# Kernel tuning notes

Hardware: AMD Instinct MI355X
Metric: run time of the kernel (lower is better)

The kernel has to match this reference:

```python
import jax, jax.numpy as jnp
import numpy as np

B, C, T = 8, 1024, 2048
CI = C // 2
BN_EPS = 1e-5


def setup_inputs() -> dict:
    key = jax.random.key(0)
    ks = jax.random.split(key, 12)
    sc_in = 1.0 / np.sqrt(C)
    sc_ci = 1.0 / np.sqrt(CI)
    return {
        "x": jax.random.normal(ks[0], (B, C, T), dtype=jnp.float32),
        "Wq_w": jax.random.normal(ks[1], (CI, C), dtype=jnp.float32) * sc_in,
        "Wq_b": jax.random.normal(ks[2], (CI,), dtype=jnp.float32) * 0.02,
        "Wk_w": jax.random.normal(ks[3], (CI, C), dtype=jnp.float32) * sc_in,
        "Wk_b": jax.random.normal(ks[4], (CI,), dtype=jnp.float32) * 0.02,
        "Wv_w": jax.random.normal(ks[5], (CI, C), dtype=jnp.float32) * sc_in,
        "Wv_b": jax.random.normal(ks[6], (CI,), dtype=jnp.float32) * 0.02,
        "Wo_w": jax.random.normal(ks[7], (C, CI), dtype=jnp.float32) * sc_ci,
        "Wo_b": jax.random.normal(ks[8], (C,), dtype=jnp.float32) * 0.02,
        "gamma": jax.random.normal(ks[9], (C,), dtype=jnp.float32) * 0.1 + 1.0,
        "beta": jax.random.normal(ks[10], (C,), dtype=jnp.float32) * 0.02,
    }


def reference(x, Wq_w, Wq_b, Wk_w, Wk_b, Wv_w, Wv_b, Wo_w, Wo_b, gamma, beta):
    # 1x1 Conv1d projections == channel-wise linear maps
    q = jnp.einsum('oc,bct->bto', Wq_w, x) + Wq_b          # [B, T, Ci]
    k = jnp.einsum('oc,bct->bot', Wk_w, x) + Wk_b[:, None]  # [B, Ci, T]
    v = jnp.einsum('oc,bct->bto', Wv_w, x) + Wv_b          # [B, T, Ci]

    s = jnp.einsum('bqc,bck->bqk', q, k)                   # [B, Tq, Tk], unscaled
    sim = jax.nn.softmax(s, axis=-2)                        # softmax over QUERY axis
    y = jnp.einsum('bqk,bkc->bcq', sim, v)                  # [B, Ci, T]

    wy = jnp.einsum('oc,bct->bot', Wo_w, y) + Wo_b[:, None]  # [B, C, T]

    # BatchNorm1d in training mode: stats over (batch, time) per channel
    mean = jnp.mean(wy, axis=(0, 2), keepdims=True)
    var = jnp.var(wy, axis=(0, 2), keepdims=True)
    wy_bn = (wy - mean) * jax.lax.rsqrt(var + BN_EPS)
    wy_bn = wy_bn * gamma[None, :, None] + beta[None, :, None]

    return wy_bn + x
```

## Files before the change

### kernel.cpp

```cpp
#include <hip/hip_runtime.h>
#include <hip/hip_fp16.h>

typedef _Float16 f16;
typedef f16 f16x8 __attribute__((ext_vector_type(8)));
typedef f16 f16x4 __attribute__((ext_vector_type(4)));
typedef float f32x4 __attribute__((ext_vector_type(4)));

constexpr int Bb = 8, Cc = 1024, Tt = 2048, Ci = 512;
constexpr float BN_EPS = 1e-5f;

__device__ __forceinline__ void gload16(const f16* g, f16* l) {
  __builtin_amdgcn_global_load_lds(
      (const __attribute__((address_space(1))) void*)g,
      (__attribute__((address_space(3))) void*)l, 16, 0, 0);
}

__global__ __launch_bounds__(256)
void cvt_kernel(const float* __restrict__ src, f16* __restrict__ dst, int n4) {
  int i = blockIdx.x * blockDim.x + threadIdx.x;
  if (i < n4) {
    float4 v = *((const float4*)src + i);
    f16x4 h;
    h[0] = (f16)v.x; h[1] = (f16)v.y; h[2] = (f16)v.z; h[3] = (f16)v.w;
    *((f16x4*)dst + i) = h;
  }
}

__global__ __launch_bounds__(256)
void cvtT_kernel(const float* __restrict__ x, f16* __restrict__ xT) {
  __shared__ float tile[64][68];
  const int b = blockIdx.z, c0 = blockIdx.y * 64, t0 = blockIdx.x * 64;
  const int tid = threadIdx.x;
  const float* xp = x + ((long)b * Cc + c0) * Tt + t0;
  {
    int r = tid >> 4, c4 = (tid & 15) * 4;
    #pragma unroll
    for (int it = 0; it < 4; it++) {
      float4 v = *(const float4*)(xp + (long)(r + it * 16) * Tt + c4);
      *(float4*)&tile[r + it * 16][c4] = v;
    }
  }
  __syncthreads();
  f16* op = xT + ((long)b * Tt + t0) * Cc + c0;
  {
    int c8 = (tid & 7) * 8;
    #pragma unroll
    for (int it = 0; it < 2; it++) {
      int t = (tid >> 3) + it * 32;
      f16x8 o;
      #pragma unroll
      for (int jj = 0; jj < 8; jj++) o[jj] = (f16)tile[c8 + jj][t];
      *(f16x8*)(op + (long)t * Cc + c8) = o;
    }
  }
}

template<int BIAS_MODE>
__global__ __launch_bounds__(512, 2)
void gemm8p(const f16* __restrict__ A, const f16* __restrict__ B,
            f16* __restrict__ C, const float* __restrict__ bias,
            int K, int lda, int ldb, int ldc, long sA, long sB, long sC)
{
  extern __shared__ f16 lds[];
  constexpr int TILE_A = 256 * 64;
  constexpr int TILE_B = 128 * 64;
  constexpr int TILE   = TILE_A + TILE_B;

  const int tid = threadIdx.x, lane = tid & 63, wv = tid >> 6;
  const int bm0 = blockIdx.y * 256, bn0 = blockIdx.x * 128;
  const int wm = (wv >> 1) * 64, wn = (wv & 1) * 64;
  const f16* Ab = A + (long)blockIdx.z * sA + (long)bm0 * lda;
  const f16* Bt = B + (long)blockIdx.z * sB + (long)bn0 * ldb;
  C += (long)blockIdx.z * sC;

  const int r16 = lane & 15, khi = lane >> 4;
  const int sw = (r16 & 7) << 4;

  auto stA = [&](int slot, int k0, int r) {
    int L = (r * 512 + tid) * 16;
    int G = L ^ (((L >> 7) & 7) << 4);
    gload16(Ab + (long)(G >> 7) * lda + k0 + ((G & 127) >> 1),
            lds + (long)slot * TILE + (r * 512 + wv * 64) * 8);
  };
  auto stB = [&](int slot, int k0, int r) {
    int L = (r * 512 + tid) * 16;
    int G = L ^ (((L >> 7) & 7) << 4);
    gload16(Bt + (long)(G >> 7) * ldb + k0 + ((G & 127) >> 1),
            lds + (long)slot * TILE + TILE_A + (r * 512 + wv * 64) * 8);
  };

  f32x4 acc[4][4] = {};
  const int nt = K >> 6;

  #pragma unroll
  for (int r = 0; r < 4; r++) stA(0, 0, r);
  #pragma unroll
  for (int r = 0; r < 2; r++) stB(0, 0, r);
  #pragma unroll
  for (int r = 0; r < 4; r++) stA(1, 64, r);
  #pragma unroll
  for (int r = 0; r < 2; r++) stB(1, 64, r);
  asm volatile("s_waitcnt vmcnt(6)" ::: "memory");
  __builtin_amdgcn_s_barrier();

  for (int t = 0; t < nt; t++) {
    const int slot = t % 3;
    const int nslot = (t + 2) % 3;
    const int k2 = (t + 2) << 6;
    const bool st = (t + 2) < nt;
    const char* baseA = (const char*)(lds + (long)slot * TILE);
    const char* baseB = (const char*)(lds + (long)slot * TILE + TILE_A);

    if (st) {
      stA(nslot, k2, 0); stA(nslot, k2, 1); stA(nslot, k2, 2); stA(nslot, k2, 3);
      stB(nslot, k2, 0); stB(nslot, k2, 1);
    }

    f16x8 af0[4], bf0[4], af1[4], bf1[4];
    #pragma unroll
    for (int mi = 0; mi < 4; mi++)
      af0[mi] = *(const f16x8*)(baseA + (((wm + mi * 16 + r16) * 128 + khi * 16) ^ sw));
    #pragma unroll
    for (int nj = 0; nj < 4; nj++)
      bf0[nj] = *(const f16x8*)(baseB + (((wn + nj * 16 + r16) * 128 + khi * 16) ^ sw));
    #pragma unroll
    for (int mi = 0; mi < 4; mi++)
      af1[mi] = *(const f16x8*)(baseA + (((wm + mi * 16 + r16) * 128 + 64 + khi * 16) ^ sw));
    #pragma unroll
    for (int nj = 0; nj < 4; nj++)
      bf1[nj] = *(const f16x8*)(baseB + (((wn + nj * 16 + r16) * 128 + 64 + khi * 16) ^ sw));

    __builtin_amdgcn_s_setprio(1);
    #pragma unroll
    for (int mi = 0; mi < 4; mi++)
      #pragma unroll
      for (int nj = 0; nj < 4; nj++)
        acc[mi][nj] = __builtin_amdgcn_mfma_f32_16x16x32_f16(af0[mi], bf0[nj], acc[mi][nj], 0, 0, 0);
    #pragma unroll
    for (int mi = 0; mi < 4; mi++)
      #pragma unroll
      for (int nj = 0; nj < 4; nj++)
        acc[mi][nj] = __builtin_amdgcn_mfma_f32_16x16x32_f16(af1[mi], bf1[nj], acc[mi][nj], 0, 0, 0);
    __builtin_amdgcn_s_setprio(0);

    __builtin_amdgcn_sched_barrier(0);
    if (st) asm volatile("s_waitcnt vmcnt(6)" ::: "memory");
    else    asm volatile("s_waitcnt vmcnt(0)" ::: "memory");
    __builtin_amdgcn_s_barrier();
  }

  const int rg = khi * 4;
  #pragma unroll
  for (int mi = 0; mi < 4; mi++) {
    const int row = bm0 + wm + mi * 16 + rg;
    #pragma unroll
    for (int nj = 0; nj < 4; nj++) {
      const int col = bn0 + wn + nj * 16 + r16;
      const float bn_ = (BIAS_MODE == 2) ? bias[col] : 0.0f;
      #pragma unroll
      for (int r = 0; r < 4; r++) {
        float v = acc[mi][nj][r] + ((BIAS_MODE == 1) ? bias[row + r] : bn_);
        C[(long)(row + r) * ldc + col] = (f16)v;
      }
    }
  }
}

__global__ __launch_bounds__(256)
void rowstat_kernel(const f16* __restrict__ S, float* __restrict__ maxs,
                    float* __restrict__ sums) {
  __shared__ float red[8];
  const int tid = threadIdx.x;
  const f16* p = S + (long)blockIdx.x * Tt;
  f16x8 v = *((const f16x8*)p + tid);
  float f[8];
  float mx = -3e38f;
  #pragma unroll
  for (int j = 0; j < 8; j++) { f[j] = (float)v[j]; mx = fmaxf(mx, f[j]); }
  #pragma unroll
  for (int off = 1; off < 64; off <<= 1) mx = fmaxf(mx, __shfl_xor(mx, off));
  const int w = tid >> 6;
  if ((tid & 63) == 0) red[w] = mx;
  __syncthreads();
  mx = fmaxf(fmaxf(red[0], red[1]), fmaxf(red[2], red[3]));
  float sum = 0.f;
  #pragma unroll
  for (int j = 0; j < 8; j++) sum += __expf(f[j] - mx);
  #pragma unroll
  for (int off = 1; off < 64; off <<= 1) sum += __shfl_xor(sum, off);
  __syncthreads();
  if ((tid & 63) == 0) red[4 + w] = sum;
  __syncthreads();
  if (tid == 0) {
    maxs[blockIdx.x] = mx;
    sums[blockIdx.x] = (red[4] + red[5]) + (red[6] + red[7]);
  }
}

__global__ __launch_bounds__(256)
void transnorm_kernel(const f16* __restrict__ St, const float* __restrict__ maxs,
                      const float* __restrict__ sums, f16* __restrict__ P) {
  __shared__ f16 tile[64][72];
  __shared__ float rm[64], ri[64];
  const int b = blockIdx.z, kt0 = blockIdx.y * 64, q0 = blockIdx.x * 64;
  const int tid = threadIdx.x;
  if (tid < 64) {
    rm[tid] = maxs[(long)b * Tt + kt0 + tid];
    ri[tid] = 1.0f / sums[(long)b * Tt + kt0 + tid];
  }
  const f16* Sp = St + ((long)b * Tt + kt0) * Tt + q0;
  {
    int r = tid >> 3, c8 = (tid & 7) * 8;
    #pragma unroll
    for (int it = 0; it < 2; it++) {
      f16x8 v = *(const f16x8*)(Sp + (long)(r + it * 32) * Tt + c8);
      *(f16x8*)&tile[r + it * 32][c8] = v;
    }
  }
  __syncthreads();
  f16* Pp = P + ((long)b * Tt + q0) * Tt + kt0;
  {
    int kt8 = (tid & 7) * 8;
    #pragma unroll
    for (int it = 0; it < 2; it++) {
      int q = (tid >> 3) + it * 32;
      f16x8 o;
      #pragma unroll
      for (int jj = 0; jj < 8; jj++) {
        int kt = kt8 + jj;
        o[jj] = (f16)(__expf((float)tile[kt][q] - rm[kt]) * ri[kt]);
      }
      *(f16x8*)(Pp + (long)q * Tt + kt8) = o;
    }
  }
}

__global__ __launch_bounds__(256)
void bnstat_kernel(const f16* __restrict__ wy, float* __restrict__ bsum,
                   float* __restrict__ bsq) {
  const int c = blockIdx.x, tid = threadIdx.x;
  float s1 = 0.f, s2 = 0.f;
  for (int b = 0; b < Bb; b++) {
    f16x8 v = *((const f16x8*)(wy + ((long)b * Cc + c) * Tt) + tid);
    #pragma unroll
    for (int jj = 0; jj < 8; jj++) { float f = (float)v[jj]; s1 += f; s2 += f * f; }
  }
  #pragma unroll
  for (int off = 1; off < 64; off <<= 1) {
    s1 += __shfl_xor(s1, off);
    s2 += __shfl_xor(s2, off);
  }
  __shared__ float l1[4], l2[4];
  const int w = tid >> 6;
  if ((tid & 63) == 0) { l1[w] = s1; l2[w] = s2; }
  __syncthreads();
  if (tid == 0) {
    bsum[c] = (l1[0] + l1[1]) + (l1[2] + l1[3]);
    bsq[c]  = (l2[0] + l2[1]) + (l2[2] + l2[3]);
  }
}

__global__ __launch_bounds__(256)
void final_kernel(const f16* __restrict__ wy, const float* __restrict__ x,
                  const float* __restrict__ gamma, const float* __restrict__ beta,
                  const float* __restrict__ bsum, const float* __restrict__ bsq,
                  float* __restrict__ out)
{
  long i = ((long)blockIdx.x * blockDim.x + threadIdx.x) * 4;
  int c = (int)((i >> 11) & (Cc - 1));
  const float cnt = (float)Bb * (float)Tt;
  float mean = bsum[c] / cnt;
  float var  = bsq[c] / cnt - mean * mean;
  float sc = rsqrtf(var + BN_EPS) * gamma[c];
  float sh = beta[c] - mean * sc;
  f16x4 w = *(const f16x4*)(wy + i);
  float4 xv = *(const float4*)(x + i);
  float4 o;
  o.x = (float)w[0] * sc + sh + xv.x;
  o.y = (float)w[1] * sc + sh + xv.y;
  o.z = (float)w[2] * sc + sh + xv.z;
  o.w = (float)w[3] * sc + sh + xv.w;
  *(float4*)(out + i) = o;
}

extern "C" void kernel_launch(void* const* d_in, const int* in_sizes, int n_in,
                              void* d_out, int out_size, void* d_ws, size_t ws_size,
                              hipStream_t stream) {
  const float* x    = (const float*)d_in[0];
  const float* Wq_w = (const float*)d_in[1];
  const float* Wq_b = (const float*)d_in[2];
  const float* Wk_w = (const float*)d_in[3];
  const float* Wk_b = (const float*)d_in[4];
  const float* Wv_w = (const float*)d_in[5];
  const float* Wv_b = (const float*)d_in[6];
  const float* Wo_w = (const float*)d_in[7];
  const float* Wo_b = (const float*)d_in[8];
  const float* gamma = (const float*)d_in[9];
  const float* beta  = (const float*)d_in[10];
  float* out = (float*)d_out;

  constexpr long SZ_XT = (long)Bb * Tt * Cc;
  constexpr long SZ_Q  = (long)Bb * Tt * Ci;
  constexpr long SZ_S  = (long)Bb * Tt * Tt;
  constexpr long SZ_W  = (long)Ci * Cc;

  f16* ws = (f16*)d_ws;
  f16* xT = ws;
  f16* P  = ws;
  f16* Qm = ws + SZ_XT;
  f16* Km = Qm + SZ_Q;
  f16* Vt = Km + SZ_Q;
  f16* St = Vt + SZ_Q;
  f16* wq = St + SZ_S;
  f16* wk = wq + SZ_W;
  f16* wv = wk + SZ_W;
  f16* wo = wv + SZ_W;
  f16* Y  = wo + SZ_W;
  f16* wy = Y + SZ_Q;
  float* maxs = (float*)(wy + SZ_XT);
  float* sums = maxs + (long)Bb * Tt;
  float* bsum = sums + (long)Bb * Tt;
  float* bsq  = bsum + Cc;

  constexpr int LDSB = (256 * 64 + 128 * 64) * 3 * 2;
  hipFuncSetAttribute(reinterpret_cast<const void*>(gemm8p<0>),
                      hipFuncAttributeMaxDynamicSharedMemorySize, LDSB);
  hipFuncSetAttribute(reinterpret_cast<const void*>(gemm8p<1>),
                      hipFuncAttributeMaxDynamicSharedMemorySize, LDSB);
  hipFuncSetAttribute(reinterpret_cast<const void*>(gemm8p<2>),
                      hipFuncAttributeMaxDynamicSharedMemorySize, LDSB);

  cvt_kernel<<<(int)(SZ_W / 4 / 256), 256, 0, stream>>>(Wq_w, wq, (int)(SZ_W / 4));
  cvt_kernel<<<(int)(SZ_W / 4 / 256), 256, 0, stream>>>(Wk_w, wk, (int)(SZ_W / 4));
  cvt_kernel<<<(int)(SZ_W / 4 / 256), 256, 0, stream>>>(Wv_w, wv, (int)(SZ_W / 4));
  cvt_kernel<<<(int)(SZ_W / 4 / 256), 256, 0, stream>>>(Wo_w, wo, (int)(SZ_W / 4));
  cvtT_kernel<<<dim3(Tt / 64, Cc / 64, Bb), 256, 0, stream>>>(x, xT);

  gemm8p<2><<<dim3(Ci / 128, Tt / 256, Bb), 512, LDSB, stream>>>(
      xT, wq, Qm, Wq_b, Cc, Cc, Cc, Ci, (long)Tt * Cc, 0, (long)Tt * Ci);
  gemm8p<2><<<dim3(Ci / 128, Tt / 256, Bb), 512, LDSB, stream>>>(
      xT, wk, Km, Wk_b, Cc, Cc, Cc, Ci, (long)Tt * Cc, 0, (long)Tt * Ci);
  gemm8p<1><<<dim3(Tt / 128, Ci / 256, Bb), 512, LDSB, stream>>>(
      wv, xT, Vt, Wv_b, Cc, Cc, Cc, Tt, 0, (long)Tt * Cc, (long)Ci * Tt);

  gemm8p<0><<<dim3(Tt / 128, Tt / 256, Bb), 512, LDSB, stream>>>(
      Km, Qm, St, nullptr, Ci, Ci, Ci, Tt, (long)Tt * Ci, (long)Tt * Ci, (long)Tt * Tt);

  rowstat_kernel<<<Bb * Tt, 256, 0, stream>>>(St, maxs, sums);
  transnorm_kernel<<<dim3(Tt / 64, Tt / 64, Bb), 256, 0, stream>>>(St, maxs, sums, P);

  gemm8p<0><<<dim3(Ci / 128, Tt / 256, Bb), 512, LDSB, stream>>>(
      P, Vt, Y, nullptr, Tt, Tt, Tt, Ci, (long)Tt * Tt, (long)Ci * Tt, (long)Tt * Ci);

  gemm8p<1><<<dim3(Tt / 128, Cc / 256, Bb), 512, LDSB, stream>>>(
      wo, Y, wy, Wo_b, Ci, Ci, Ci, Tt, 0, (long)Tt * Ci, (long)Cc * Tt);

  bnstat_kernel<<<Cc, 256, 0, stream>>>(wy, bsum, bsq);
  final_kernel<<<(int)(SZ_XT / 4 / 256), 256, 0, stream>>>(
      wy, x, gamma, beta, bsum, bsq, out);
}
```

Before: 300.6 us.

## Fuse softmax stats and BN stats into GEMM epilogues, merge Q/K projection

Computes S as Q·K^T so softmax over the query axis becomes per-column. The column max is produced by atomics in the GEMM epilogue, and a column-sum kernel exponentiates S in place. Normalisation moves onto V through a per-key scale instead of a separate transpose-normalise pass. The Q and K projections are merged into one GEMM, BatchNorm sums are accumulated with atomics in the output-projection epilogue, and blocks are remapped for XCD locality. Together these remove the rowstat, transnorm and bnstat passes and their extra traffic over the large S matrix, at the cost of atomic contention and a strided column-walking pass.

```diff
diff --git a/kernel.cpp b/kernel.cpp
--- a/kernel.cpp
+++ b/kernel.cpp
@@ -55,23 +55,32 @@
   }
 }
 
-template<int BIAS_MODE>
+template<int BIAS_MODE, bool DO_MAX, bool DO_BN>
 __global__ __launch_bounds__(512, 2)
 void gemm8p(const f16* __restrict__ A, const f16* __restrict__ B,
             f16* __restrict__ C, const float* __restrict__ bias,
-            int K, int lda, int ldb, int ldc, long sA, long sB, long sC)
+            unsigned* __restrict__ gmax, float* __restrict__ bnsum,
+            float* __restrict__ bnsq,
+            int K, int lda, int ldb, int ldc, long sA, long sB, long sC,
+            int nx, int ny)
 {
   extern __shared__ f16 lds[];
   constexpr int TILE_A = 256 * 64;
   constexpr int TILE_B = 128 * 64;
   constexpr int TILE   = TILE_A + TILE_B;
 
+  const int per = gridDim.x >> 3;
+  const int nid = (blockIdx.x & 7) * per + (blockIdx.x >> 3);
+  const int bz = nid / (nx * ny);
+  const int rem = nid - bz * nx * ny;
+  const int by = rem / nx, bx = rem - by * nx;
+
   const int tid = threadIdx.x, lane = tid & 63, wv = tid >> 6;
-  const int bm0 = blockIdx.y * 256, bn0 = blockIdx.x * 128;
+  const int bm0 = by * 256, bn0 = bx * 128;
   const int wm = (wv >> 1) * 64, wn = (wv & 1) * 64;
-  const f16* Ab = A + (long)blockIdx.z * sA + (long)bm0 * lda;
-  const f16* Bt = B + (long)blockIdx.z * sB + (long)bn0 * ldb;
-  C += (long)blockIdx.z * sC;
+  const f16* Ab = A + (long)bz * sA + (long)bm0 * lda;
+  const f16* Bt = B + (long)bz * sB + (long)bn0 * ldb;
+  C += (long)bz * sC;
 
   const int r16 = lane & 15, khi = lane >> 4;
   const int sw = (r16 & 7) << 4;
@@ -118,29 +127,24 @@
 
     f16x8 af0[4], bf0[4], af1[4], bf1[4];
     #pragma unroll
-    for (int mi = 0; mi < 4; mi++)
-      af0[mi] = *(const f16x8*)(baseA + (((wm + mi * 16 + r16) * 128 + khi * 16) ^ sw));
-    #pragma unroll
-    for (int nj = 0; nj < 4; nj++)
-      bf0[nj] = *(const f16x8*)(baseB + (((wn + nj * 16 + r16) * 128 + khi * 16) ^ sw));
-    #pragma unroll
-    for (int mi = 0; mi < 4; mi++)
-      af1[mi] = *(const f16x8*)(baseA + (((wm + mi * 16 + r16) * 128 + 64 + khi * 16) ^ sw));
-    #pragma unroll
-    for (int nj = 0; nj < 4; nj++)
-      bf1[nj] = *(const f16x8*)(baseB + (((wn + nj * 16 + r16) * 128 + 64 + khi * 16) ^ sw));
+    for (int i = 0; i < 4; i++) {
+      af0[i] = *(const f16x8*)(baseA + (((wm + i * 16 + r16) * 128 + khi * 16) ^ sw));
+      af1[i] = *(const f16x8*)(baseA + (((wm + i * 16 + r16) * 128 + 64 + khi * 16) ^ sw));
+    }
+    #pragma unroll
+    for (int j = 0; j < 4; j++) {
+      bf0[j] = *(const f16x8*)(baseB + (((wn + j * 16 + r16) * 128 + khi * 16) ^ sw));
+      bf1[j] = *(const f16x8*)(baseB + (((wn + j * 16 + r16) * 128 + 64 + khi * 16) ^ sw));
+    }
 
     __builtin_amdgcn_s_setprio(1);
     #pragma unroll
-    for (int mi = 0; mi < 4; mi++)
+    for (int i = 0; i < 4; i++)
       #pragma unroll
-      for (int nj = 0; nj < 4; nj++)
-        acc[mi][nj] = __builtin_amdgcn_mfma_f32_16x16x32_f16(af0[mi], bf0[nj], acc[mi][nj], 0, 0, 0);
-    #pragma unroll
-    for (int mi = 0; mi < 4; mi++)
-      #pragma unroll
-      for (int nj = 0; nj < 4; nj++)
-        acc[mi][nj] = __builtin_amdgcn_mfma_f32_16x16x32_f16(af1[mi], bf1[nj], acc[mi][nj], 0, 0, 0);
+      for (int j = 0; j < 4; j++) {
+        acc[i][j] = __builtin_amdgcn_mfma_f32_16x16x32_f16(af0[i], bf0[j], acc[i][j], 0, 0, 0);
+        acc[i][j] = __builtin_amdgcn_mfma_f32_16x16x32_f16(af1[i], bf1[j], acc[i][j], 0, 0, 0);
+      }
     __builtin_amdgcn_s_setprio(0);
 
     __builtin_amdgcn_sched_barrier(0);
@@ -150,114 +154,80 @@
   }
 
   const int rg = khi * 4;
-  #pragma unroll
-  for (int mi = 0; mi < 4; mi++) {
-    const int row = bm0 + wm + mi * 16 + rg;
-    #pragma unroll
-    for (int nj = 0; nj < 4; nj++) {
-      const int col = bn0 + wn + nj * 16 + r16;
-      const float bn_ = (BIAS_MODE == 2) ? bias[col] : 0.0f;
+  float cmx[4] = {-3e38f, -3e38f, -3e38f, -3e38f};
+  #pragma unroll
+  for (int i = 0; i < 4; i++) {
+    const int row0 = bm0 + wm + i * 16 + rg;
+    #pragma unroll
+    for (int r = 0; r < 4; r++) {
+      const int row = row0 + r;
+      const float br = (BIAS_MODE == 1) ? bias[row] : 0.0f;
+      float s1 = 0.f, s2 = 0.f;
       #pragma unroll
-      for (int r = 0; r < 4; r++) {
-        float v = acc[mi][nj][r] + ((BIAS_MODE == 1) ? bias[row + r] : bn_);
-        C[(long)(row + r) * ldc + col] = (f16)v;
+      for (int j = 0; j < 4; j++) {
+        const int col = bn0 + wn + j * 16 + r16;
+        float v = acc[i][j][r] + ((BIAS_MODE == 2) ? bias[col] : br);
+        C[(long)row * ldc + col] = (f16)v;
+        if (DO_MAX) cmx[j] = fmaxf(cmx[j], v);
+        if (DO_BN) { s1 += v; s2 += v * v; }
       }
-    }
-  }
-}
-
-__global__ __launch_bounds__(256)
-void rowstat_kernel(const f16* __restrict__ S, float* __restrict__ maxs,
-                    float* __restrict__ sums) {
-  __shared__ float red[8];
-  const int tid = threadIdx.x;
-  const f16* p = S + (long)blockIdx.x * Tt;
-  f16x8 v = *((const f16x8*)p + tid);
-  float f[8];
-  float mx = -3e38f;
-  #pragma unroll
-  for (int j = 0; j < 8; j++) { f[j] = (float)v[j]; mx = fmaxf(mx, f[j]); }
-  #pragma unroll
-  for (int off = 1; off < 64; off <<= 1) mx = fmaxf(mx, __shfl_xor(mx, off));
-  const int w = tid >> 6;
-  if ((tid & 63) == 0) red[w] = mx;
-  __syncthreads();
-  mx = fmaxf(fmaxf(red[0], red[1]), fmaxf(red[2], red[3]));
-  float sum = 0.f;
-  #pragma unroll
-  for (int j = 0; j < 8; j++) sum += __expf(f[j] - mx);
-  #pragma unroll
-  for (int off = 1; off < 64; off <<= 1) sum += __shfl_xor(sum, off);
-  __syncthreads();
-  if ((tid & 63) == 0) red[4 + w] = sum;
-  __syncthreads();
-  if (tid == 0) {
-    maxs[blockIdx.x] = mx;
-    sums[blockIdx.x] = (red[4] + red[5]) + (red[6] + red[7]);
-  }
-}
-
-__global__ __launch_bounds__(256)
-void transnorm_kernel(const f16* __restrict__ St, const float* __restrict__ maxs,
-                      const float* __restrict__ sums, f16* __restrict__ P) {
-  __shared__ f16 tile[64][72];
-  __shared__ float rm[64], ri[64];
-  const int b = blockIdx.z, kt0 = blockIdx.y * 64, q0 = blockIdx.x * 64;
-  const int tid = threadIdx.x;
-  if (tid < 64) {
-    rm[tid] = maxs[(long)b * Tt + kt0 + tid];
-    ri[tid] = 1.0f / sums[(long)b * Tt + kt0 + tid];
-  }
-  const f16* Sp = St + ((long)b * Tt + kt0) * Tt + q0;
-  {
-    int r = tid >> 3, c8 = (tid & 7) * 8;
-    #pragma unroll
-    for (int it = 0; it < 2; it++) {
-      f16x8 v = *(const f16x8*)(Sp + (long)(r + it * 32) * Tt + c8);
-      *(f16x8*)&tile[r + it * 32][c8] = v;
-    }
-  }
-  __syncthreads();
-  f16* Pp = P + ((long)b * Tt + q0) * Tt + kt0;
-  {
-    int kt8 = (tid & 7) * 8;
-    #pragma unroll
-    for (int it = 0; it < 2; it++) {
-      int q = (tid >> 3) + it * 32;
-      f16x8 o;
-      #pragma unroll
-      for (int jj = 0; jj < 8; jj++) {
-        int kt = kt8 + jj;
-        o[jj] = (f16)(__expf((float)tile[kt][q] - rm[kt]) * ri[kt]);
+      if (DO_BN) {
+        #pragma unroll
+        for (int off = 1; off < 16; off <<= 1) {
+          s1 += __shfl_xor(s1, off);
+          s2 += __shfl_xor(s2, off);
+        }
+        if (r16 == 0) { atomicAdd(bnsum + row, s1); atomicAdd(bnsq + row, s2); }
       }
-      *(f16x8*)(Pp + (long)q * Tt + kt8) = o;
-    }
-  }
-}
-
-__global__ __launch_bounds__(256)
-void bnstat_kernel(const f16* __restrict__ wy, float* __restrict__ bsum,
-                   float* __restrict__ bsq) {
-  const int c = blockIdx.x, tid = threadIdx.x;
-  float s1 = 0.f, s2 = 0.f;
-  for (int b = 0; b < Bb; b++) {
-    f16x8 v = *((const f16x8*)(wy + ((long)b * Cc + c) * Tt) + tid);
-    #pragma unroll
-    for (int jj = 0; jj < 8; jj++) { float f = (float)v[jj]; s1 += f; s2 += f * f; }
-  }
-  #pragma unroll
-  for (int off = 1; off < 64; off <<= 1) {
-    s1 += __shfl_xor(s1, off);
-    s2 += __shfl_xor(s2, off);
-  }
-  __shared__ float l1[4], l2[4];
-  const int w = tid >> 6;
-  if ((tid & 63) == 0) { l1[w] = s1; l2[w] = s2; }
-  __syncthreads();
-  if (tid == 0) {
-    bsum[c] = (l1[0] + l1[1]) + (l1[2] + l1[3]);
-    bsq[c]  = (l2[0] + l2[1]) + (l2[2] + l2[3]);
-  }
+    }
+  }
+  if (DO_MAX) {
+    #pragma unroll
+    for (int j = 0; j < 4; j++) {
+      float mx = cmx[j];
+      mx = fmaxf(mx, __shfl_xor(mx, 16));
+      mx = fmaxf(mx, __shfl_xor(mx, 32));
+      if (khi == 0) {
+        const int col = bn0 + wn + j * 16 + r16;
+        unsigned u = __float_as_uint(mx);
+        unsigned key = (u & 0x80000000u) ? ~u : (u | 0x80000000u);
+        atomicMax(gmax + (long)bz * ldc + col, key);
+      }
+    }
+  }
+}
+
+__global__ __launch_bounds__(256)
+void colsum_kernel(f16* __restrict__ E, const unsigned* __restrict__ gmax,
+                   float* __restrict__ sums) {
+  const int b = blockIdx.z;
+  const int kt = blockIdx.x * 256 + threadIdx.x;
+  const long q0 = (long)blockIdx.y * 128;
+  unsigned key = gmax[b * Tt + kt];
+  float m = (key & 0x80000000u) ? __uint_as_float(key ^ 0x80000000u)
+                                : __uint_as_float(~key);
+  f16* p = E + ((long)b * Tt + q0) * Tt + kt;
+  float s = 0.f;
+  #pragma unroll 4
+  for (int q = 0; q < 128; q++) {
+    float e = __expf((float)p[(long)q * Tt] - m);
+    p[(long)q * Tt] = (f16)e;
+    s += e;
+  }
+  atomicAdd(sums + b * Tt + kt, s);
+}
+
+__global__ __launch_bounds__(256)
+void vscale_kernel(f16* __restrict__ Vt, const float* __restrict__ sums) {
+  long i = ((long)blockIdx.x * 256 + threadIdx.x) * 8;
+  int kt = (int)(i & (Tt - 1));
+  int b = (int)(i >> 20);
+  f16x8 v = *(f16x8*)(Vt + i);
+  const float* sp = sums + b * Tt + kt;
+  #pragma unroll
+  for (int j = 0; j < 8; j++)
+    v[j] = (f16)((float)v[j] * __fdividef(1.0f, sp[j]));
+  *(f16x8*)(Vt + i) = v;
 }
 
 __global__ __launch_bounds__(256)
@@ -305,57 +275,67 @@
   constexpr long SZ_W  = (long)Ci * Cc;
 
   f16* ws = (f16*)d_ws;
-  f16* xT = ws;
-  f16* P  = ws;
-  f16* Qm = ws + SZ_XT;
-  f16* Km = Qm + SZ_Q;
-  f16* Vt = Km + SZ_Q;
-  f16* St = Vt + SZ_Q;
-  f16* wq = St + SZ_S;
-  f16* wk = wq + SZ_W;
-  f16* wv = wk + SZ_W;
-  f16* wo = wv + SZ_W;
-  f16* Y  = wo + SZ_W;
-  f16* wy = Y + SZ_Q;
-  float* maxs = (float*)(wy + SZ_XT);
-  float* sums = maxs + (long)Bb * Tt;
+  f16* xT  = ws;
+  f16* QK  = xT + SZ_XT;
+  f16* Vt  = QK + SZ_XT;
+  f16* Sq  = Vt + SZ_Q;
+  f16* Y   = Sq + SZ_S;
+  f16* wy  = Y + SZ_Q;
+  f16* wqk = wy + SZ_XT;
+  f16* wv  = wqk + 2 * SZ_W;
+  f16* wo  = wv + SZ_W;
+  unsigned* gmax = (unsigned*)(wo + SZ_W);
+  float* sums = (float*)(gmax + (long)Bb * Tt);
   float* bsum = sums + (long)Bb * Tt;
   float* bsq  = bsum + Cc;
+  float* qkb  = bsq + Cc;
 
   constexpr int LDSB = (256 * 64 + 128 * 64) * 3 * 2;
-  hipFuncSetAttribute(reinterpret_cast<const void*>(gemm8p<0>),
-                      hipFuncAttributeMaxDynamicSharedMemorySize, LDSB);
-  hipFuncSetAttribute(reinterpret_cast<const void*>(gemm8p<1>),
-                      hipFuncAttributeMaxDynamicSharedMemorySize, LDSB);
-  hipFuncSetAttribute(reinterpret_cast<const void*>(gemm8p<2>),
-                      hipFuncAttributeMaxDynamicSharedMemorySize, LDSB);
-
-  cvt_kernel<<<(int)(SZ_W / 4 / 256), 256, 0, stream>>>(Wq_w, wq, (int)(SZ_W / 4));
-  cvt_kernel<<<(int)(SZ_W / 4 / 256), 256, 0, stream>>>(Wk_w, wk, (int)(SZ_W / 4));
+  hipFuncSetAttribute(reinterpret_cast<const void*>(gemm8p<2, false, false>),
+                      hipFuncAttributeMaxDynamicSharedMemorySize, LDSB);
+  hipFuncSetAttribute(reinterpret_cast<const void*>(gemm8p<1, false, false>),
+                      hipFuncAttributeMaxDynamicSharedMemorySize, LDSB);
+  hipFuncSetAttribute(reinterpret_cast<const void*>(gemm8p<0, true, false>),
+                      hipFuncAttributeMaxDynamicSharedMemorySize, LDSB);
+  hipFuncSetAttribute(reinterpret_cast<const void*>(gemm8p<0, false, false>),
+                      hipFuncAttributeMaxDynamicSharedMemorySize, LDSB);
+  hipFuncSetAttribute(reinterpret_cast<const void*>(gemm8p<1, false, true>),
+                      hipFuncAttributeMaxDynamicSharedMemorySize, LDSB);
+
+  hipMemsetAsync(gmax, 0, ((long)Bb * Tt * 2 + 2 * Cc) * sizeof(float), stream);
+  hipMemcpyAsync(qkb, Wq_b, Ci * sizeof(float), hipMemcpyDeviceToDevice, stream);
+  hipMemcpyAsync(qkb + Ci, Wk_b, Ci * sizeof(float), hipMemcpyDeviceToDevice, stream);
+
+  cvt_kernel<<<(int)(SZ_W / 4 / 256), 256, 0, stream>>>(Wq_w, wqk, (int)(SZ_W / 4));
+  cvt_kernel<<<(int)(SZ_W / 4 / 256), 256, 0, stream>>>(Wk_w, wqk + SZ_W, (int)(SZ_W / 4));
   cvt_kernel<<<(int)(SZ_W / 4 / 256), 256, 0, stream>>>(Wv_w, wv, (int)(SZ_W / 4));
   cvt_kernel<<<(int)(SZ_W / 4 / 256), 256, 0, stream>>>(Wo_w, wo, (int)(SZ_W / 4));
   cvtT_kernel<<<dim3(Tt / 64, Cc / 64, Bb), 256, 0, stream>>>(x, xT);
 
-  gemm8p<2><<<dim3(Ci / 128, Tt / 256, Bb), 512, LDSB, stream>>>(
-      xT, wq, Qm, Wq_b, Cc, Cc, Cc, Ci, (long)Tt * Cc, 0, (long)Tt * Ci);
-  gemm8p<2><<<dim3(Ci / 128, Tt / 256, Bb), 512, LDSB, stream>>>(
-      xT, wk, Km, Wk_b, Cc, Cc, Cc, Ci, (long)Tt * Cc, 0, (long)Tt * Ci);
-  gemm8p<1><<<dim3(Tt / 128, Ci / 256, Bb), 512, LDSB, stream>>>(
-      wv, xT, Vt, Wv_b, Cc, Cc, Cc, Tt, 0, (long)Tt * Cc, (long)Ci * Tt);
-
-  gemm8p<0><<<dim3(Tt / 128, Tt / 256, Bb), 512, LDSB, stream>>>(
-      Km, Qm, St, nullptr, Ci, Ci, Ci, Tt, (long)Tt * Ci, (long)Tt * Ci, (long)Tt * Tt);
-
-  rowstat_kernel<<<Bb * Tt, 256, 0, stream>>>(St, maxs, sums);
-  transnorm_kernel<<<dim3(Tt / 64, Tt / 64, Bb), 256, 0, stream>>>(St, maxs, sums, P);
-
-  gemm8p<0><<<dim3(Ci / 128, Tt / 256, Bb), 512, LDSB, stream>>>(
-      P, Vt, Y, nullptr, Tt, Tt, Tt, Ci, (long)Tt * Tt, (long)Ci * Tt, (long)Tt * Ci);
-
-  gemm8p<1><<<dim3(Tt / 128, Cc / 256, Bb), 512, LDSB, stream>>>(
-      wo, Y, wy, Wo_b, Ci, Ci, Ci, Tt, 0, (long)Tt * Ci, (long)Cc * Tt);
-
-  bnstat_kernel<<<Cc, 256, 0, stream>>>(wy, bsum, bsq);
+  gemm8p<2, false, false><<<8 * 8 * Bb, 512, LDSB, stream>>>(
+      xT, wqk, QK, qkb, nullptr, nullptr, nullptr,
+      Cc, Cc, Cc, 1024, (long)Tt * Cc, 0, (long)Tt * 1024, 8, 8);
+
+  gemm8p<1, false, false><<<16 * 2 * Bb, 512, LDSB, stream>>>(
+      wv, xT, Vt, Wv_b, nullptr, nullptr, nullptr,
+      Cc, Cc, Cc, Tt, 0, (long)Tt * Cc, (long)Ci * Tt, 16, 2);
+
+  gemm8p<0, true, false><<<16 * 8 * Bb, 512, LDSB, stream>>>(
+      QK, QK + 512, Sq, nullptr, gmax, nullptr, nullptr,
+      Ci, 1024, 1024, Tt, (long)Tt * 1024, (long)Tt * 1024, (long)Tt * Tt, 16, 8);
+
+  colsum_kernel<<<dim3(Tt / 256, Tt / 128, Bb), 256, 0, stream>>>(Sq, gmax, sums);
+
+  vscale_kernel<<<(int)(SZ_Q / 8 / 256), 256, 0, stream>>>(Vt, sums);
+
+  gemm8p<0, false, false><<<4 * 8 * Bb, 512, LDSB, stream>>>(
+      Sq, Vt, Y, nullptr, nullptr, nullptr, nullptr,
+      Tt, Tt, Tt, Ci, (long)Tt * Tt, (long)Ci * Tt, (long)Tt * Ci, 4, 8);
+
+  gemm8p<1, false, true><<<16 * 4 * Bb, 512, LDSB, stream>>>(
+      wo, Y, wy, Wo_b, nullptr, bsum, bsq,
+      Ci, Ci, Ci, Tt, 0, (long)Tt * Ci, (long)Cc * Tt, 16, 4);
+
   final_kernel<<<(int)(SZ_XT / 4 / 256), 256, 0, stream>>>(
       wy, x, gamma, beta, bsum, bsq, out);
 }
```

Measured after the change: 333.6 us. +11.0%, slower.
